# Kernel tuning notes

Hardware: AMD Instinct MI355X
Metric: run time of the kernel (lower is better)

Reference implementation:

```python
import jax, jax.numpy as jnp
import numpy as np
from math import sqrt

H = 16
D_MODEL = 1024
D_K = D_MODEL // H
B, S = 2, 2048


def setup_inputs() -> dict:
    key = jax.random.key(0)
    ks = jax.random.split(key, 12)
    scale = 1.0 / sqrt(D_MODEL)
    inp = {
        "query": jax.random.normal(ks[0], (B, S, D_MODEL), jnp.float32),
        "key": jax.random.normal(ks[1], (B, S, D_MODEL), jnp.float32),
        "value": jax.random.normal(ks[2], (B, S, D_MODEL), jnp.float32),
        # causal mask [B, S, S]; module unsqueezes head dim itself
        "mask": jnp.broadcast_to(jnp.tril(jnp.ones((S, S), jnp.int32)), (B, S, S)),
        "Wq": jax.random.normal(ks[3], (D_MODEL, D_MODEL), jnp.float32) * scale,
        "bq": jnp.zeros((D_MODEL,), jnp.float32),
        "Wk": jax.random.normal(ks[4], (D_MODEL, D_MODEL), jnp.float32) * scale,
        "bk": jnp.zeros((D_MODEL,), jnp.float32),
        "Wv": jax.random.normal(ks[5], (D_MODEL, D_MODEL), jnp.float32) * scale,
        "bv": jnp.zeros((D_MODEL,), jnp.float32),
        "Wo": jax.random.normal(ks[6], (D_MODEL, D_MODEL), jnp.float32) * scale,
        "bo": jnp.zeros((D_MODEL,), jnp.float32),
    }
    return inp


def reference(query, key, value, mask, Wq, bq, Wk, bk, Wv, bv, Wo, bo):
    nb = query.shape[0]

    def proj(x, W, b):
        # nn.Linear: x @ W.T + b, then split heads -> [B, H, S, D_K]
        y = jnp.einsum('bsd,ed->bse', x, W) + b
        return y.reshape(nb, -1, H, D_K).transpose(0, 2, 1, 3)

    q = proj(query, Wq, bq)
    k = proj(key, Wk, bk)
    v = proj(value, Wv, bv)

    scores = jnp.einsum('bhqd,bhkd->bhqk', q, k) / sqrt(D_K)  # [B,H,S,S]
    scores = jnp.where(mask[:, None, :, :] == 0, -jnp.inf, scores)
    probs = jax.nn.softmax(scores, axis=-1)  # dropout in eval mode (identity)
    ctx = jnp.einsum('bhqk,bhkd->bhqd', probs, v)
    ctx = ctx.transpose(0, 2, 1, 3).reshape(nb, -1, H * D_K)
    return jnp.einsum('bsd,ed->bse', ctx, Wo) + bo
```

## Files before the change

kernel.cpp:

```cpp
#include <hip/hip_runtime.h>
#include <hip/hip_bf16.h>
#include <stdint.h>


#define H_ 16
#define DM 1024
#define DK_ 64
#define BB 2
#define SS 2048
#define PSTR 72

typedef __bf16 bf16x8 __attribute__((ext_vector_type(8)));
typedef __bf16 bf16x2_t __attribute__((ext_vector_type(2)));
typedef float f32x4 __attribute__((ext_vector_type(4)));

#define GLOAD_LDS16(g, l)                                            \
  __builtin_amdgcn_global_load_lds(                                  \
      (__attribute__((address_space(1))) void*)(g),                  \
      (__attribute__((address_space(3))) void*)(l), 16, 0, 0)

__device__ __forceinline__ unsigned short f2bf_u(float f) {
  unsigned int u = __float_as_uint(f);
  u += 0x7fffu + ((u >> 16) & 1u);
  return (unsigned short)(u >> 16);
}

__device__ __forceinline__ unsigned int pack_bf16(float a, float b) {
#if __has_builtin(__builtin_amdgcn_cvt_pk_bf16_f32)
  bf16x2_t v = __builtin_amdgcn_cvt_pk_bf16_f32(a, b);
  unsigned int u;
  __builtin_memcpy(&u, &v, 4);
  return u;
#else
  return (unsigned int)f2bf_u(a) | ((unsigned int)f2bf_u(b) << 16);
#endif
}

__device__ __forceinline__ float fexp2(float x) {
#if __has_builtin(__builtin_amdgcn_exp2f)
  return __builtin_amdgcn_exp2f(x);
#else
  return exp2f(x);
#endif
}

struct Cvt {
  const float* s[7];
  unsigned short* d[7];
  int n[7];
};

__global__ __launch_bounds__(256) void convert_kernel(Cvt c) {
  const int y = blockIdx.y;
  const float* __restrict__ src = c.s[y];
  unsigned short* __restrict__ dst = c.d[y];
  const int nv = c.n[y] >> 2;
  for (int i = blockIdx.x * 256 + threadIdx.x; i < nv; i += 1024 * 256) {
    float4 v = *(const float4*)(src + (size_t)i * 4);
    ushort4 o;
    o.x = f2bf_u(v.x); o.y = f2bf_u(v.y); o.z = f2bf_u(v.z); o.w = f2bf_u(v.w);
    *(ushort4*)(dst + (size_t)i * 4) = o;
  }
}

__global__ __launch_bounds__(512, 2) void qkv_gemm(
    const unsigned short* Qi, const unsigned short* Ki, const unsigned short* Vi,
    const unsigned short* Wq, const unsigned short* Wk, const unsigned short* Wv,
    const float* bq, const float* bk, const float* bv,
    unsigned short* Qf, unsigned short* Kf, unsigned short* Vf) {
  __shared__ unsigned short As[2 * 2 * 16 * 512];
  __shared__ unsigned short Bs[2 * 2 * 16 * 512];
  const int p = blockIdx.x;
  const int c = p & 7, idx = p >> 3;
  const int x = idx & 3, yy = (idx >> 2) & 1, z = idx >> 3;
  const int y = c * 2 + yy;
  const int m0 = y * 256, n0 = x * 256;
  const unsigned short* A = z == 0 ? Qi : (z == 1 ? Ki : Vi);
  const unsigned short* W = z == 0 ? Wq : (z == 1 ? Wk : Wv);
  const float* bias = z == 0 ? bq : (z == 1 ? bk : bv);
  const float scale = z == 0 ? 0.1803368801111204f : 1.0f;

  const int tid = threadIdx.x;
  const int wave = tid >> 6, lane = tid & 63;
  const int lm = lane & 15, quad = lane >> 4;
  const int wr = wave >> 2, wc = wave & 3;

  const int scs = 8 * ((lane & 3) ^ ((lane >> 3) & 3));
  const size_t asrc0 = (size_t)(m0 + wave * 16 + (lane >> 2)) * DM + scs;
  const size_t bsrc0 = (size_t)(n0 + wave * 16 + (lane >> 2)) * DM + scs;
  const int sdst = wave * 512 + lane * 8;

  const int rcol = (quad * 8) ^ (((lm >> 1) & 3) * 8);
  const int aoff = wr * 8 * 512 + lm * 32 + rcol;
  const int boff = wc * 4 * 512 + lm * 32 + rcol;

  f32x4 acc[8][4];
#pragma unroll
  for (int i = 0; i < 8; ++i)
#pragma unroll
    for (int j = 0; j < 4; ++j) {
      f32x4 zz = {0.f, 0.f, 0.f, 0.f};
      acc[i][j] = zz;
    }

  auto stA = [&](int buf, int kh, int kt) {
    const unsigned short* s = A + asrc0 + (size_t)kt * 64 + kh * 32;
    unsigned short* d = As + buf * 16384 + kh * 8192 + sdst;
    GLOAD_LDS16(s, d);
    GLOAD_LDS16(s + (size_t)128 * DM, d + 4096);
  };
  auto stB = [&](int buf, int kh, int kt) {
    const unsigned short* s = W + bsrc0 + (size_t)kt * 64 + kh * 32;
    unsigned short* d = Bs + buf * 16384 + kh * 8192 + sdst;
    GLOAD_LDS16(s, d);
    GLOAD_LDS16(s + (size_t)128 * DM, d + 4096);
  };

  stA(0, 0, 0); stB(0, 0, 0); stA(0, 1, 0); stB(0, 1, 0);
  stA(1, 0, 1); stB(1, 0, 1); stA(1, 1, 1);
  asm volatile("s_waitcnt vmcnt(6)" ::: "memory");
  __builtin_amdgcn_s_barrier();

#define BARR __builtin_amdgcn_s_barrier()
#define SCHB __builtin_amdgcn_sched_barrier(0)
#define MFMA8(AF, B0_, B1_, J0, J1)                                          \
  __builtin_amdgcn_s_setprio(1);                                             \
  _Pragma("unroll")                                                          \
  for (int i = 0; i < 8; ++i) {                                              \
    acc[i][J0] = __builtin_amdgcn_mfma_f32_16x16x32_bf16(AF[i], B0_,         \
                                                         acc[i][J0], 0, 0, 0); \
    acc[i][J1] = __builtin_amdgcn_mfma_f32_16x16x32_bf16(AF[i], B1_,         \
                                                         acc[i][J1], 0, 0, 0); \
  }                                                                          \
  __builtin_amdgcn_s_setprio(0)

#pragma unroll 2
  for (int t = 0; t < 14; ++t) {
    const int buf = t & 1;
    const unsigned short* Ab = As + buf * 16384;
    const unsigned short* Bb = Bs + buf * 16384;
    bf16x8 a0[8], b0[4];
#pragma unroll
    for (int i = 0; i < 8; ++i)
      a0[i] = *(const bf16x8*)(Ab + aoff + i * 512);
#pragma unroll
    for (int j = 0; j < 4; ++j)
      b0[j] = *(const bf16x8*)(Bb + boff + j * 512);
    stB(buf ^ 1, 1, t + 1);
    BARR; SCHB;
    MFMA8(a0, b0[0], b0[1], 0, 1);
    SCHB; BARR;
    stA(buf, 0, t + 2);
    BARR; SCHB;
    MFMA8(a0, b0[2], b0[3], 2, 3);
    SCHB; BARR;
    bf16x8 a1[8], b1[4];
#pragma unroll
    for (int i = 0; i < 8; ++i)
      a1[i] = *(const bf16x8*)(Ab + 8192 + aoff + i * 512);
#pragma unroll
    for (int j = 0; j < 4; ++j)
      b1[j] = *(const bf16x8*)(Bb + 8192 + boff + j * 512);
    stB(buf, 0, t + 2);
    BARR; SCHB;
    MFMA8(a1, b1[0], b1[1], 0, 1);
    SCHB; BARR;
    stA(buf, 1, t + 2);
    asm volatile("s_waitcnt vmcnt(6)" ::: "memory");
    BARR; SCHB;
    MFMA8(a1, b1[2], b1[3], 2, 3);
    SCHB; BARR;
  }

  stB(1, 1, 15);
  asm volatile("s_waitcnt vmcnt(0)" ::: "memory");
  __builtin_amdgcn_s_barrier();
#pragma unroll
  for (int tt = 0; tt < 2; ++tt) {
    const unsigned short* Ab = As + tt * 16384;
    const unsigned short* Bb = Bs + tt * 16384;
#pragma unroll
    for (int kh = 0; kh < 2; ++kh) {
      bf16x8 a2[8], b2[4];
#pragma unroll
      for (int i = 0; i < 8; ++i)
        a2[i] = *(const bf16x8*)(Ab + kh * 8192 + aoff + i * 512);
#pragma unroll
      for (int j = 0; j < 4; ++j)
        b2[j] = *(const bf16x8*)(Bb + kh * 8192 + boff + j * 512);
#pragma unroll
      for (int i = 0; i < 8; ++i)
#pragma unroll
        for (int j = 0; j < 4; ++j)
          acc[i][j] = __builtin_amdgcn_mfma_f32_16x16x32_bf16(
              a2[i], b2[j], acc[i][j], 0, 0, 0);
    }
  }
#undef MFMA8
#undef SCHB
#undef BARR

  if (z == 2) {
#pragma unroll
    for (int j = 0; j < 4; ++j) {
      int gn = n0 + wc * 64 + j * 16 + lm;
      float bv_ = bias[gn];
      int h2 = gn >> 6, dk = gn & 63;
      int a = dk >> 4, ln = dk & 15;
#pragma unroll
      for (int i = 0; i < 8; ++i) {
        int s0 = m0 + wr * 128 + i * 16 + quad * 4;
        int b2 = s0 >> 11, sl = s0 & 2047;
        int kt2 = sl >> 6, cc2 = (sl >> 5) & 1, qk = (sl >> 3) & 3, j0 = sl & 7;
        size_t base =
            ((size_t)(((b2 * 16 + h2) * 32 + kt2) * 4 + a) * 2 + cc2) * 512 +
            (qk * 16 + ln) * 8 + j0;
        uint2 w;
        w.x = pack_bf16(acc[i][j][0] + bv_, acc[i][j][1] + bv_);
        w.y = pack_bf16(acc[i][j][2] + bv_, acc[i][j][3] + bv_);
        *(uint2*)(Vf + base) = w;
      }
    }
  } else {
    unsigned short* out = z == 0 ? Qf : Kf;
#pragma unroll
    for (int j = 0; j < 4; ++j) {
      int gn = n0 + wc * 64 + j * 16 + lm;
      float bv_ = bias[gn];
      int h2 = gn >> 6, d64 = gn & 63;
      int cc2 = (d64 >> 5) & 1, qk = (d64 >> 3) & 3, jjq = d64 & 7;
#pragma unroll
      for (int i = 0; i < 8; ++i)
#pragma unroll
        for (int r = 0; r < 4; ++r) {
          int gm = m0 + wr * 128 + i * 16 + quad * 4 + r;
          int b2 = gm >> 11, sl = gm & 2047;
          size_t base =
              ((size_t)((b2 * 16 + h2) * 128 + (sl >> 4)) * 2 + cc2) * 512 +
              (qk * 16 + (sl & 15)) * 8 + jjq;
          out[base] = f2bf_u((acc[i][j][r] + bv_) * scale);
        }
    }
  }
}

__global__ __launch_bounds__(256) void o_gemm(
    const unsigned short* Ctx, const unsigned short* Wo, const float* bo,
    float* out) {
  __shared__ unsigned short As[2 * 2 * 8 * 512];
  __shared__ unsigned short Bs[2 * 2 * 4 * 512];
  const int p = blockIdx.x;
  const int c = p & 7, j0 = p >> 3;
  const int x = j0 & 15, yy = j0 >> 4;
  const int y = c * 4 + yy;
  const int m0 = y * 128, n0 = x * 64;
  const int tid = threadIdx.x;
  const int wave = tid >> 6, lane = tid & 63;
  const int lm = lane & 15, quad = lane >> 4;
  const int wm = (wave >> 1) * 64, wn = (wave & 1) * 32;

  const int scs = 8 * ((lane & 3) ^ ((lane >> 3) & 3));
  const int srow = lane >> 2;
  const size_t aSrc0 = (size_t)(m0 + wave * 32 + srow) * DM + scs;
  const size_t bSrc0 = (size_t)(n0 + wave * 16 + srow) * DM + scs;
  const int aDst0 = wave * 2 * 512 + lane * 8;
  const int bDst0 = wave * 512 + lane * 8;

  const int rcol = (quad * 8) ^ (((lm >> 1) & 3) * 8);
  const int aoff = (wm >> 4) * 512 + lm * 32 + rcol;
  const int boff = (wn >> 4) * 512 + lm * 32 + rcol;

  f32x4 acc[4][2];
#pragma unroll
  for (int i = 0; i < 4; ++i)
#pragma unroll
    for (int j = 0; j < 2; ++j) {
      f32x4 z = {0.f, 0.f, 0.f, 0.f};
      acc[i][j] = z;
    }

  auto stAB = [&](int buf, int kt) {
#pragma unroll
    for (int kh = 0; kh < 2; ++kh) {
      const unsigned short* sa = Ctx + aSrc0 + (size_t)kt * 64 + kh * 32;
      unsigned short* da = As + buf * 8192 + kh * 4096 + aDst0;
      GLOAD_LDS16(sa, da);
      GLOAD_LDS16(sa + (size_t)16 * DM, da + 512);
      const unsigned short* sb = Wo + bSrc0 + (size_t)kt * 64 + kh * 32;
      GLOAD_LDS16(sb, Bs + buf * 4096 + kh * 2048 + bDst0);
    }
  };

  stAB(0, 0);
  for (int kt = 0; kt < DM / 64; ++kt) {
    __syncthreads();
    const int buf = kt & 1;
    if (kt + 1 < DM / 64) stAB(buf ^ 1, kt + 1);
    const unsigned short* Ac = As + buf * 8192;
    const unsigned short* Bc = Bs + buf * 4096;
#pragma unroll
    for (int kh = 0; kh < 2; ++kh) {
      bf16x8 af[4], bf_[2];
#pragma unroll
      for (int i = 0; i < 4; ++i)
        af[i] = *(const bf16x8*)(Ac + kh * 4096 + aoff + i * 512);
#pragma unroll
      for (int j = 0; j < 2; ++j)
        bf_[j] = *(const bf16x8*)(Bc + kh * 2048 + boff + j * 512);
#pragma unroll
      for (int i = 0; i < 4; ++i)
#pragma unroll
        for (int j = 0; j < 2; ++j)
          acc[i][j] = __builtin_amdgcn_mfma_f32_16x16x32_bf16(
              af[i], bf_[j], acc[i][j], 0, 0, 0);
    }
  }

#pragma unroll
  for (int j = 0; j < 2; ++j) {
    int gn = n0 + wn + j * 16 + lm;
    float bv_ = bo[gn];
#pragma unroll
    for (int i = 0; i < 4; ++i)
#pragma unroll
      for (int r = 0; r < 4; ++r) {
        int gm = m0 + wm + i * 16 + quad * 4 + r;
        out[(size_t)gm * DM + gn] = acc[i][j][r] + bv_;
      }
  }
}

__global__ __launch_bounds__(256, 2) void attn_kernel(
    const unsigned short* __restrict__ Qf, const unsigned short* __restrict__ Kf,
    const unsigned short* __restrict__ Vf, unsigned short* __restrict__ Ctx) {
  __shared__ float Rs[4][64][21];
  __shared__ unsigned short Ps[4][16 * PSTR];
  const int p = blockIdx.x;
  const int bh = p & 31, qt = 31 - (p >> 5);
  const int b = bh >> 4, h = bh & 15;
  const int tid = threadIdx.x, wave = tid >> 6, lane = tid & 63;
  const int lm = lane & 15, quad = lane >> 4;

  const int qbase0 = qt * 64;
  const int nkw = qt + 1;

  const unsigned short* Kb = Kf + (size_t)bh * 256 * 512;
  const unsigned short* Vb = Vf + (size_t)bh * 256 * 512;
  unsigned short* Pw = Ps[wave];

  bf16x8 onesf;
  {
    unsigned short ob[8] = {0x3F80, 0x3F80, 0x3F80, 0x3F80,
                            0x3F80, 0x3F80, 0x3F80, 0x3F80};
    __builtin_memcpy(&onesf, ob, 16);
  }

  bf16x8 qf[4][2];
#pragma unroll
  for (int f = 0; f < 4; ++f)
#pragma unroll
    for (int c = 0; c < 2; ++c)
      qf[f][c] = *(const bf16x8*)(Qf +
          ((size_t)(bh * 128 + qt * 4 + f) * 2 + c) * 512 + lane * 8);

  f32x4 oacc[4][4];
#pragma unroll
  for (int f = 0; f < 4; ++f)
#pragma unroll
    for (int a = 0; a < 4; ++a) {
      f32x4 z = {0.f, 0.f, 0.f, 0.f};
      oacc[f][a] = z;
    }
  f32x4 lacc[4];
#pragma unroll
  for (int f = 0; f < 4; ++f) {
    f32x4 z = {0.f, 0.f, 0.f, 0.f};
    lacc[f] = z;
  }

  auto loadK = [&](bf16x8 (&kf)[4][2], int kt) {
#pragma unroll
    for (int ik = 0; ik < 4; ++ik)
#pragma unroll
      for (int c = 0; c < 2; ++c)
        kf[ik][c] = *(const bf16x8*)(Kb +
            ((size_t)(kt * 4 + ik) * 2 + c) * 512 + lane * 8);
  };

  auto computeKt = [&](bf16x8 (&kf)[4][2], int kt, bool last) {
    bf16x8 vf[4][2];
#pragma unroll
    for (int a = 0; a < 4; ++a)
#pragma unroll
      for (int c = 0; c < 2; ++c)
        vf[a][c] = *(const bf16x8*)(Vb +
            ((size_t)(kt * 8 + a * 2 + c)) * 512 + lane * 8);

#pragma unroll
    for (int f = 0; f < 4; ++f) {
      f32x4 s[4];
#pragma unroll
      for (int ik = 0; ik < 4; ++ik) {
        f32x4 zz = {0.f, 0.f, 0.f, 0.f};
        zz = __builtin_amdgcn_mfma_f32_16x16x32_bf16(kf[ik][0], qf[f][0], zz,
                                                     0, 0, 0);
        s[ik] = __builtin_amdgcn_mfma_f32_16x16x32_bf16(kf[ik][1], qf[f][1],
                                                        zz, 0, 0, 0);
      }
      if (last) {
        int qg = qbase0 + f * 16 + lm;
#pragma unroll
        for (int ik = 0; ik < 4; ++ik)
#pragma unroll
          for (int r = 0; r < 4; ++r) {
            int kg = kt * 64 + ik * 16 + quad * 4 + r;
            if (kg > qg) s[ik][r] = -1e30f;
          }
      }
#pragma unroll
      for (int ik = 0; ik < 4; ++ik) {
        float p0 = fexp2(s[ik][0]);
        float p1 = fexp2(s[ik][1]);
        float p2 = fexp2(s[ik][2]);
        float p3 = fexp2(s[ik][3]);
        uint2 w;
        w.x = pack_bf16(p0, p1);
        w.y = pack_bf16(p2, p3);
        *(uint2*)(Pw + lm * PSTR + ik * 16 + quad * 4) = w;
      }
      bf16x8 pf[2];
#pragma unroll
      for (int c = 0; c < 2; ++c)
        pf[c] = *(const bf16x8*)(Pw + lm * PSTR + c * 32 + quad * 8);
#pragma unroll
      for (int a = 0; a < 4; ++a) {
        oacc[f][a] = __builtin_amdgcn_mfma_f32_16x16x32_bf16(pf[0], vf[a][0],
                                                             oacc[f][a], 0, 0, 0);
        oacc[f][a] = __builtin_amdgcn_mfma_f32_16x16x32_bf16(pf[1], vf[a][1],
                                                             oacc[f][a], 0, 0, 0);
      }
      lacc[f] = __builtin_amdgcn_mfma_f32_16x16x32_bf16(pf[0], onesf, lacc[f],
                                                        0, 0, 0);
      lacc[f] = __builtin_amdgcn_mfma_f32_16x16x32_bf16(pf[1], onesf, lacc[f],
                                                        0, 0, 0);
    }
  };

  bf16x8 kA[4][2], kB[4][2];
  if (wave < nkw) loadK(kA, wave);
  for (int kt = wave; kt < nkw; kt += 8) {
    if (kt + 4 < nkw) loadK(kB, kt + 4);
    computeKt(kA, kt, kt == nkw - 1);
    if (kt + 4 < nkw) {
      if (kt + 8 < nkw) loadK(kA, kt + 8);
      computeKt(kB, kt + 4, kt + 4 == nkw - 1);
    }
  }

  const size_t obase = (size_t)(b * SS) * DM + (size_t)h * DK_;
#pragma unroll
  for (int f = 0; f < 4; ++f) {
    __syncthreads();
#pragma unroll
    for (int a = 0; a < 4; ++a)
#pragma unroll
      for (int r = 0; r < 4; ++r)
        Rs[wave][lane][a * 4 + r] = oacc[f][a][r];
#pragma unroll
    for (int r = 0; r < 4; ++r)
      Rs[wave][lane][16 + r] = lacc[f][r];
    __syncthreads();
#pragma unroll
    for (int r = 0; r < 4; ++r) {
      float ov = Rs[0][lane][wave * 4 + r] + Rs[1][lane][wave * 4 + r] +
                 Rs[2][lane][wave * 4 + r] + Rs[3][lane][wave * 4 + r];
      float lv = Rs[0][lane][16 + r] + Rs[1][lane][16 + r] +
                 Rs[2][lane][16 + r] + Rs[3][lane][16 + r];
      int qg = qbase0 + f * 16 + quad * 4 + r;
      Ctx[obase + (size_t)qg * DM + wave * 16 + lm] = f2bf_u(ov / lv);
    }
  }
}

extern "C" void kernel_launch(void* const* d_in, const int* in_sizes, int n_in,
                              void* d_out, int out_size, void* d_ws, size_t ws_size,
                              hipStream_t stream) {
  const float* q = (const float*)d_in[0];
  const float* k = (const float*)d_in[1];
  const float* v = (const float*)d_in[2];
  const float* Wq = (const float*)d_in[4];
  const float* bq = (const float*)d_in[5];
  const float* Wk = (const float*)d_in[6];
  const float* bk = (const float*)d_in[7];
  const float* Wv = (const float*)d_in[8];
  const float* bv = (const float*)d_in[9];
  const float* Wo = (const float*)d_in[10];
  const float* bo = (const float*)d_in[11];

  const size_t NX = (size_t)BB * SS * DM;
  const size_t NW = (size_t)DM * DM;
  unsigned short* ws = (unsigned short*)d_ws;
  unsigned short* Qi = ws;
  unsigned short* Ki = Qi + NX;
  unsigned short* Vi = Ki + NX;
  unsigned short* Wqb = Vi + NX;
  unsigned short* Wkb = Wqb + NW;
  unsigned short* Wvb = Wkb + NW;
  unsigned short* Wob = Wvb + NW;
  unsigned short* Qfr = Wob + NW;
  unsigned short* Kfr = Qfr + NX;
  unsigned short* Vfr = Kfr + NX;
  unsigned short* Ctx = Vfr + NX;

  Cvt c;
  c.s[0] = q; c.s[1] = k; c.s[2] = v; c.s[3] = Wq; c.s[4] = Wk; c.s[5] = Wv; c.s[6] = Wo;
  c.d[0] = Qi; c.d[1] = Ki; c.d[2] = Vi; c.d[3] = Wqb; c.d[4] = Wkb; c.d[5] = Wvb; c.d[6] = Wob;
  c.n[0] = c.n[1] = c.n[2] = (int)NX;
  c.n[3] = c.n[4] = c.n[5] = c.n[6] = (int)NW;

  convert_kernel<<<dim3(1024, 7), dim3(256), 0, stream>>>(c);
  qkv_gemm<<<dim3(192), dim3(512), 0, stream>>>(Qi, Ki, Vi, Wqb, Wkb, Wvb,
                                                bq, bk, bv, Qfr, Kfr, Vfr);
  attn_kernel<<<dim3(1024), dim3(256), 0, stream>>>(Qfr, Kfr, Vfr, Ctx);
  o_gemm<<<dim3(512), dim3(256), 0, stream>>>(Ctx, Wob, bo, (float*)d_out);
}
```

Before: 226.9 us.

## Double-buffer attention P tiles to interleave QK/exp with PV; relax GEMM vmcnt waits

The attention inner loop now keeps two per-wave P staging buffers in LDS. It software-pipelines the four query fragments so the QK^T MFMAs and exp/pack of the next fragment overlap with the PV MFMAs of the previous one. Separately, the projection GEMM loop adds an earlier partial vmcnt wait and loosens the later one (6 to 8), spreading the wait for global-to-LDS loads. The changes trade more LDS and register pressure, plus finer-grained synchronisation that must still hold, for less serialisation between dependent MFMA chains.

```diff
diff --git a/kernel.cpp b/kernel.cpp
--- a/kernel.cpp
+++ b/kernel.cpp
@@ -151,6 +151,7 @@
     MFMA8(a0, b0[0], b0[1], 0, 1);
     SCHB; BARR;
     stA(buf, 0, t + 2);
+    asm volatile("s_waitcnt vmcnt(10)" ::: "memory");
     BARR; SCHB;
     MFMA8(a0, b0[2], b0[3], 2, 3);
     SCHB; BARR;
@@ -166,7 +167,7 @@
     MFMA8(a1, b1[0], b1[1], 0, 1);
     SCHB; BARR;
     stA(buf, 1, t + 2);
-    asm volatile("s_waitcnt vmcnt(6)" ::: "memory");
+    asm volatile("s_waitcnt vmcnt(8)" ::: "memory");
     BARR; SCHB;
     MFMA8(a1, b1[2], b1[3], 2, 3);
     SCHB; BARR;
@@ -334,7 +335,7 @@
     const unsigned short* __restrict__ Qf, const unsigned short* __restrict__ Kf,
     const unsigned short* __restrict__ Vf, unsigned short* __restrict__ Ctx) {
   __shared__ float Rs[4][64][21];
-  __shared__ unsigned short Ps[4][16 * PSTR];
+  __shared__ unsigned short Ps[4][2][16 * PSTR];
   const int p = blockIdx.x;
   const int bh = p & 31, qt = 31 - (p >> 5);
   const int b = bh >> 4, h = bh & 15;
@@ -346,7 +347,8 @@
 
   const unsigned short* Kb = Kf + (size_t)bh * 256 * 512;
   const unsigned short* Vb = Vf + (size_t)bh * 256 * 512;
-  unsigned short* Pw = Ps[wave];
+  unsigned short* Pw0 = Ps[wave][0];
+  unsigned short* Pw1 = Ps[wave][1];
 
   bf16x8 onesf;
   {
@@ -387,6 +389,57 @@
             ((size_t)(kt * 4 + ik) * 2 + c) * 512 + lane * 8);
   };
 
+  auto qk = [&](f32x4 (&s)[4], bf16x8 (&kf)[4][2], int f) {
+#pragma unroll
+    for (int ik = 0; ik < 4; ++ik) {
+      f32x4 zz = {0.f, 0.f, 0.f, 0.f};
+      zz = __builtin_amdgcn_mfma_f32_16x16x32_bf16(kf[ik][0], qf[f][0], zz,
+                                                   0, 0, 0);
+      s[ik] = __builtin_amdgcn_mfma_f32_16x16x32_bf16(kf[ik][1], qf[f][1], zz,
+                                                      0, 0, 0);
+    }
+  };
+  auto maskS = [&](f32x4 (&s)[4], int kt, int f) {
+    int qg = qbase0 + f * 16 + lm;
+#pragma unroll
+    for (int ik = 0; ik < 4; ++ik)
+#pragma unroll
+      for (int r = 0; r < 4; ++r) {
+        int kg = kt * 64 + ik * 16 + quad * 4 + r;
+        if (kg > qg) s[ik][r] = -1e30f;
+      }
+  };
+  auto expPack = [&](f32x4 (&s)[4], unsigned short* dst) {
+#pragma unroll
+    for (int ik = 0; ik < 4; ++ik) {
+      float p0 = fexp2(s[ik][0]);
+      float p1 = fexp2(s[ik][1]);
+      float p2 = fexp2(s[ik][2]);
+      float p3 = fexp2(s[ik][3]);
+      uint2 w;
+      w.x = pack_bf16(p0, p1);
+      w.y = pack_bf16(p2, p3);
+      *(uint2*)(dst + lm * PSTR + ik * 16 + quad * 4) = w;
+    }
+  };
+  auto pv = [&](int f, const unsigned short* src, bf16x8 (&vf)[4][2]) {
+    bf16x8 pf[2];
+#pragma unroll
+    for (int c = 0; c < 2; ++c)
+      pf[c] = *(const bf16x8*)(src + lm * PSTR + c * 32 + quad * 8);
+#pragma unroll
+    for (int a = 0; a < 4; ++a) {
+      oacc[f][a] = __builtin_amdgcn_mfma_f32_16x16x32_bf16(pf[0], vf[a][0],
+                                                           oacc[f][a], 0, 0, 0);
+      oacc[f][a] = __builtin_amdgcn_mfma_f32_16x16x32_bf16(pf[1], vf[a][1],
+                                                           oacc[f][a], 0, 0, 0);
+    }
+    lacc[f] = __builtin_amdgcn_mfma_f32_16x16x32_bf16(pf[0], onesf, lacc[f],
+                                                      0, 0, 0);
+    lacc[f] = __builtin_amdgcn_mfma_f32_16x16x32_bf16(pf[1], onesf, lacc[f],
+                                                      0, 0, 0);
+  };
+
   auto computeKt = [&](bf16x8 (&kf)[4][2], int kt, bool last) {
     bf16x8 vf[4][2];
 #pragma unroll
@@ -396,54 +449,19 @@
         vf[a][c] = *(const bf16x8*)(Vb +
             ((size_t)(kt * 8 + a * 2 + c)) * 512 + lane * 8);
 
-#pragma unroll
-    for (int f = 0; f < 4; ++f) {
-      f32x4 s[4];
-#pragma unroll
-      for (int ik = 0; ik < 4; ++ik) {
-        f32x4 zz = {0.f, 0.f, 0.f, 0.f};
-        zz = __builtin_amdgcn_mfma_f32_16x16x32_bf16(kf[ik][0], qf[f][0], zz,
-                                                     0, 0, 0);
-        s[ik] = __builtin_amdgcn_mfma_f32_16x16x32_bf16(kf[ik][1], qf[f][1],
-                                                        zz, 0, 0, 0);
-      }
-      if (last) {
-        int qg = qbase0 + f * 16 + lm;
-#pragma unroll
-        for (int ik = 0; ik < 4; ++ik)
-#pragma unroll
-          for (int r = 0; r < 4; ++r) {
-            int kg = kt * 64 + ik * 16 + quad * 4 + r;
-            if (kg > qg) s[ik][r] = -1e30f;
-          }
-      }
-#pragma unroll
-      for (int ik = 0; ik < 4; ++ik) {
-        float p0 = fexp2(s[ik][0]);
-        float p1 = fexp2(s[ik][1]);
-        float p2 = fexp2(s[ik][2]);
-        float p3 = fexp2(s[ik][3]);
-        uint2 w;
-        w.x = pack_bf16(p0, p1);
-        w.y = pack_bf16(p2, p3);
-        *(uint2*)(Pw + lm * PSTR + ik * 16 + quad * 4) = w;
-      }
-      bf16x8 pf[2];
-#pragma unroll
-      for (int c = 0; c < 2; ++c)
-        pf[c] = *(const bf16x8*)(Pw + lm * PSTR + c * 32 + quad * 8);
-#pragma unroll
-      for (int a = 0; a < 4; ++a) {
-        oacc[f][a] = __builtin_amdgcn_mfma_f32_16x16x32_bf16(pf[0], vf[a][0],
-                                                             oacc[f][a], 0, 0, 0);
-        oacc[f][a] = __builtin_amdgcn_mfma_f32_16x16x32_bf16(pf[1], vf[a][1],
-                                                             oacc[f][a], 0, 0, 0);
-      }
-      lacc[f] = __builtin_amdgcn_mfma_f32_16x16x32_bf16(pf[0], onesf, lacc[f],
-                                                        0, 0, 0);
-      lacc[f] = __builtin_amdgcn_mfma_f32_16x16x32_bf16(pf[1], onesf, lacc[f],
-                                                        0, 0, 0);
-    }
+    f32x4 sa[4], sb[4];
+    qk(sa, kf, 0); if (last) maskS(sa, kt, 0);
+    expPack(sa, Pw0);
+    qk(sb, kf, 1); if (last) maskS(sb, kt, 1);
+    expPack(sb, Pw1);
+    pv(0, Pw0, vf);
+    qk(sa, kf, 2); if (last) maskS(sa, kt, 2);
+    expPack(sa, Pw0);
+    pv(1, Pw1, vf);
+    qk(sb, kf, 3); if (last) maskS(sb, kt, 3);
+    expPack(sb, Pw1);
+    pv(2, Pw0, vf);
+    pv(3, Pw1, vf);
   };
 
   bf16x8 kA[4][2], kB[4][2];
```

Result: no change. 224.5 us, median of 2 (-1.0%).
